# Optimization experiments

Hardware: AMD Instinct MI355X
Metric: run time of the kernel (lower is better)

## Reference

```python
import jax, jax.numpy as jnp
import numpy as np

N = 50000       # nodes
E = 800000      # edges
IN = 128        # in_channels
HID = 64        # hidden_channels
OUT = 32        # out_channels
H = 4           # heads
EH = 64         # edge_hidden_channels
EOUT = 2        # edge_out_channels
NEG_SLOPE = 0.2 # PyG GATConv default


def gat_conv(x, edge_index, W, att_src, att_dst, bias, num_nodes):
    """PyG GATConv, concat=False, add_self_loops=False, eval mode (no dropout).
    edge_attr is ignored because edge_dim=None (lin_edge is None in PyG).
    Returns (out [N, C], alpha [E, H])."""
    heads, C = att_src.shape
    xl = (x @ W).reshape(-1, heads, C)                 # [N, H, C]
    src, dst = edge_index[0], edge_index[1]
    a_src = jnp.sum(xl * att_src, axis=-1)             # [N, H]
    a_dst = jnp.sum(xl * att_dst, axis=-1)             # [N, H]
    alpha = jax.nn.leaky_relu(a_src[src] + a_dst[dst], NEG_SLOPE)  # [E, H]
    # segment softmax over destination nodes
    amax = jax.ops.segment_max(alpha, dst, num_segments=num_nodes)
    amax = jnp.where(jnp.isfinite(amax), amax, 0.0)
    ex = jnp.exp(alpha - amax[dst])
    denom = jax.ops.segment_sum(ex, dst, num_segments=num_nodes)
    alpha_n = ex / (denom[dst] + 1e-16)                # [E, H]
    msg = xl[src] * alpha_n[:, :, None]                # [E, H, C]
    out = jax.ops.segment_sum(msg, dst, num_segments=num_nodes)  # [N, H, C]
    out = out.mean(axis=1) + bias                      # concat=False -> head mean
    return out, alpha_n


def setup_inputs() -> dict:
    key = jax.random.key(0)
    ks = jax.random.split(key, 16)
    x = jax.random.normal(ks[0], (N, IN), dtype=jnp.float32)
    edge_index = jax.random.randint(ks[1], (2, E), 0, N, dtype=jnp.int32)
    edge_attr = jax.random.normal(ks[2], (E, 5), dtype=jnp.float32)
    s = lambda fan: 1.0 / np.sqrt(fan)
    W1 = jax.random.normal(ks[3], (IN, H * HID), dtype=jnp.float32) * s(IN)
    att1_src = jax.random.normal(ks[4], (H, HID), dtype=jnp.float32) * s(HID)
    att1_dst = jax.random.normal(ks[5], (H, HID), dtype=jnp.float32) * s(HID)
    b1 = jnp.zeros((HID,), dtype=jnp.float32)
    W3 = jax.random.normal(ks[6], (HID, H * OUT), dtype=jnp.float32) * s(HID)
    att3_src = jax.random.normal(ks[7], (H, OUT), dtype=jnp.float32) * s(OUT)
    att3_dst = jax.random.normal(ks[8], (H, OUT), dtype=jnp.float32) * s(OUT)
    b3 = jnp.zeros((OUT,), dtype=jnp.float32)
    EIN = 2 * OUT + H  # cat(out_src, alpha, out_dst)
    mW1 = jax.random.normal(ks[9], (EIN, EH), dtype=jnp.float32) * s(EIN)
    mb1 = jnp.zeros((EH,), dtype=jnp.float32)
    mW2 = jax.random.normal(ks[10], (EH, EOUT), dtype=jnp.float32) * s(EH)
    mb2 = jnp.zeros((EOUT,), dtype=jnp.float32)
    return {"x": x, "edge_index": edge_index, "edge_attr": edge_attr,
            "return_attention_weights": 1,
            "W1": W1, "att1_src": att1_src, "att1_dst": att1_dst, "b1": b1,
            "W3": W3, "att3_src": att3_src, "att3_dst": att3_dst, "b3": b3,
            "mW1": mW1, "mb1": mb1, "mW2": mW2, "mb2": mb2}


def reference(x, edge_index, edge_attr, return_attention_weights,
              W1, att1_src, att1_dst, b1, W3, att3_src, att3_dst, b3,
              mW1, mb1, mW2, mb2):
    edge_len = edge_attr.shape[0]  # == E (no self loops added)
    out, alpha = gat_conv(x, edge_index, W1, att1_src, att1_dst, b1, N)
    out, alpha = gat_conv(out, edge_index, W3, att3_src, att3_dst, b3, N)
    # F.dropout with training=False is the identity (eval mode)
    ei = edge_index[:, :edge_len]
    al = alpha[:edge_len, :]
    out_src = out[ei[0]]                                # [E, OUT]
    out_dst = out[ei[1]]                                # [E, OUT]
    edge_feat = jnp.concatenate([out_src, al, out_dst], axis=-1)  # [E, 2*OUT+H]
    h = jax.nn.relu(edge_feat @ mW1 + mb1)
    edge_out = h @ mW2 + mb2                            # [E, EOUT]
    return (out, edge_out)
```

## Files before the change

kernel.cpp:

```cpp
#include <hip/hip_runtime.h>
#include <hip/hip_fp16.h>

constexpr int NN   = 50000;
constexpr int EE   = 800000;
constexpr int INF  = 128;
constexpr int NH   = 4;

struct __align__(8) h4 { __half2 a, b; };

__device__ __forceinline__ float elw(float a) {
    a = (a > 0.f) ? a : 0.2f * a;
    return __expf(a);
}

__global__ __launch_bounds__(256) void gemm_pq_half(const float* __restrict__ A,
                                                    const float* __restrict__ B,
                                                    __half* __restrict__ C,
                                                    int N, int K, int M) {
    __shared__ float As[16][68];
    __shared__ float Bs[16][64];
    const int tid = threadIdx.x;
    const int tx = tid & 15, ty = tid >> 4;
    const int row0 = blockIdx.x * 64, col0 = blockIdx.y * 64;

    float acc[4][4] = {};

    for (int k0 = 0; k0 < K; k0 += 16) {
        {
            const int a_row = tid >> 2;
            const int a_k   = (tid & 3) * 4;
            const int gr    = row0 + a_row;
            float4 v = make_float4(0.f, 0.f, 0.f, 0.f);
            if (gr < N) v = *(const float4*)(A + (size_t)gr * K + k0 + a_k);
            As[a_k + 0][a_row] = v.x;
            As[a_k + 1][a_row] = v.y;
            As[a_k + 2][a_row] = v.z;
            As[a_k + 3][a_row] = v.w;
        }
        {
            const int b_k = tid >> 4;
            const int b_c = (tid & 15) * 4;
            float4 w = *(const float4*)(B + (size_t)(k0 + b_k) * M + col0 + b_c);
            *(float4*)&Bs[b_k][b_c] = w;
        }
        __syncthreads();
        #pragma unroll
        for (int kk = 0; kk < 16; ++kk) {
            float4 a = *(const float4*)&As[kk][ty * 4];
            float4 b = *(const float4*)&Bs[kk][tx * 4];
            const float av[4] = {a.x, a.y, a.z, a.w};
            const float bv[4] = {b.x, b.y, b.z, b.w};
            #pragma unroll
            for (int i = 0; i < 4; ++i)
                #pragma unroll
                for (int j = 0; j < 4; ++j)
                    acc[i][j] = fmaf(av[i], bv[j], acc[i][j]);
        }
        __syncthreads();
    }
    #pragma unroll
    for (int i = 0; i < 4; ++i) {
        const int r = row0 + ty * 4 + i;
        if (r < N) {
            __half* cp = C + (size_t)r * M + col0 + tx * 4;
            __half2 q0 = __halves2half2(__float2half_rn(acc[i][0]), __float2half_rn(acc[i][1]));
            __half2 q1 = __halves2half2(__float2half_rn(acc[i][2]), __float2half_rn(acc[i][3]));
            *(__half2*)cp       = q0;
            *(__half2*)(cp + 2) = q1;
        }
    }
}

template <int CH, bool HOUT>
__global__ __launch_bounds__(256) void gemm_att(const float* __restrict__ A,
                                                const float* __restrict__ B,
                                                void* __restrict__ Cv,
                                                const float* __restrict__ att_s,
                                                const float* __restrict__ att_d,
                                                float* __restrict__ a_s,
                                                float* __restrict__ a_d,
                                                int N, int K, int M) {
    __shared__ float As[16][68];
    __shared__ float Bs[16][64];
    const int tid = threadIdx.x;
    const int tx = tid & 15, ty = tid >> 4;
    const int row0 = blockIdx.x * 64, col0 = blockIdx.y * 64;

    const int col  = col0 + tx * 4;
    const int head = col / CH;
    const int pos  = col % CH;
    float attS[4], attD[4];
    #pragma unroll
    for (int j = 0; j < 4; ++j) {
        attS[j] = att_s[head * CH + pos + j];
        attD[j] = att_d[head * CH + pos + j];
    }

    float acc[4][4] = {};

    for (int k0 = 0; k0 < K; k0 += 16) {
        {
            const int a_row = tid >> 2;
            const int a_k   = (tid & 3) * 4;
            const int gr    = row0 + a_row;
            float4 v = make_float4(0.f, 0.f, 0.f, 0.f);
            if (gr < N) v = *(const float4*)(A + (size_t)gr * K + k0 + a_k);
            As[a_k + 0][a_row] = v.x;
            As[a_k + 1][a_row] = v.y;
            As[a_k + 2][a_row] = v.z;
            As[a_k + 3][a_row] = v.w;
        }
        {
            const int b_k = tid >> 4;
            const int b_c = (tid & 15) * 4;
            float4 w = *(const float4*)(B + (size_t)(k0 + b_k) * M + col0 + b_c);
            *(float4*)&Bs[b_k][b_c] = w;
        }
        __syncthreads();
        #pragma unroll
        for (int kk = 0; kk < 16; ++kk) {
            float4 a = *(const float4*)&As[kk][ty * 4];
            float4 b = *(const float4*)&Bs[kk][tx * 4];
            const float av[4] = {a.x, a.y, a.z, a.w};
            const float bv[4] = {b.x, b.y, b.z, b.w};
            #pragma unroll
            for (int i = 0; i < 4; ++i)
                #pragma unroll
                for (int j = 0; j < 4; ++j)
                    acc[i][j] = fmaf(av[i], bv[j], acc[i][j]);
        }
        __syncthreads();
    }
    #pragma unroll
    for (int i = 0; i < 4; ++i) {
        const int r = row0 + ty * 4 + i;
        if (r < N) {
            if constexpr (HOUT) {
                __half* C  = (__half*)Cv;
                __half* cp = C + (size_t)r * M + col0 + tx * 4;
                __half2 q0 = __halves2half2(__float2half_rn(acc[i][0]), __float2half_rn(acc[i][1]));
                __half2 q1 = __halves2half2(__float2half_rn(acc[i][2]), __float2half_rn(acc[i][3]));
                *(__half2*)cp       = q0;
                *(__half2*)(cp + 2) = q1;
            } else {
                float* C  = (float*)Cv;
                float* cp = C + (size_t)r * M + col0 + tx * 4;
                cp[0] = acc[i][0]; cp[1] = acc[i][1]; cp[2] = acc[i][2]; cp[3] = acc[i][3];
            }
        }
        float ss = 0.f, sd = 0.f;
        #pragma unroll
        for (int j = 0; j < 4; ++j) {
            ss = fmaf(acc[i][j], attS[j], ss);
            sd = fmaf(acc[i][j], attD[j], sd);
        }
        #pragma unroll
        for (int msk = 1; msk < CH / 4; msk <<= 1) {
            ss += __shfl_xor(ss, msk, 64);
            sd += __shfl_xor(sd, msk, 64);
        }
        if ((tx & (CH / 4 - 1)) == 0 && r < N) {
            a_s[r * NH + head] = ss;
            a_d[r * NH + head] = sd;
        }
    }
}

__global__ __launch_bounds__(256) void count_deg_k(const int* __restrict__ ei,
                                                   int* __restrict__ deg) {
    const int e = blockIdx.x * 256 + threadIdx.x;
    if (e < EE) atomicAdd(&deg[ei[EE + e]], 1);
}

__global__ __launch_bounds__(1024) void scan_k(const int* __restrict__ deg,
                                               int* __restrict__ rowptr,
                                               int* __restrict__ cursor) {
    __shared__ int wsum[16];
    const int tid = threadIdx.x;
    const int lane = tid & 63, wv = tid >> 6;
    int total = 0;
    for (int base = 0; base < NN; base += 1024) {
        const int i = base + tid;
        const int v = (i < NN) ? deg[i] : 0;
        int incl = v;
        #pragma unroll
        for (int d = 1; d < 64; d <<= 1) {
            int t = __shfl_up(incl, d, 64);
            if (lane >= d) incl += t;
        }
        if (lane == 63) wsum[wv] = incl;
        __syncthreads();
        if (wv == 0) {
            int s = (lane < 16) ? wsum[lane] : 0;
            #pragma unroll
            for (int d = 1; d < 16; d <<= 1) {
                int t = __shfl_up(s, d, 64);
                if (lane >= d) s += t;
            }
            if (lane < 16) wsum[lane] = s;
        }
        __syncthreads();
        const int excl = total + (wv > 0 ? wsum[wv - 1] : 0) + incl - v;
        const int chunk = wsum[15];
        if (i < NN) { rowptr[i] = excl; cursor[i] = excl; }
        total += chunk;
        __syncthreads();
    }
    if (tid == 0) rowptr[NN] = total;
}

__global__ __launch_bounds__(256) void scatter_perm_k(const int* __restrict__ ei,
                                                      int* __restrict__ cursor,
                                                      int* __restrict__ perm,
                                                      int* __restrict__ psrc,
                                                      int* __restrict__ pdst) {
    const int e = blockIdx.x * 256 + threadIdx.x;
    if (e >= EE) return;
    const int d = ei[EE + e];
    const int p = atomicAdd(&cursor[d], 1);
    perm[p] = e;
    psrc[p] = ei[e];
    pdst[p] = d;
}

__global__ __launch_bounds__(256) void softagg1h(const int* __restrict__ rowptr,
                                                 const int* __restrict__ psrc,
                                                 const float* __restrict__ a_s,
                                                 const float* __restrict__ a_d,
                                                 const __half* __restrict__ xl,
                                                 const float* __restrict__ bias,
                                                 float* __restrict__ out) {
    const int wv = threadIdx.x >> 6, lane = threadIdx.x & 63;
    const int n = blockIdx.x * 4 + wv;
    if (n >= NN) return;
    const int r0 = rowptr[n], r1 = rowptr[n + 1];
    const int hh = lane >> 4;
    const float ad = a_d[n * NH + hh];

    const h4* X = (const h4*)xl;
    float4 A0 = {0,0,0,0}, A1 = {0,0,0,0}, A2 = {0,0,0,0}, A3 = {0,0,0,0};
    float sum = 0.f;
    int j = r0;
    for (; j + 7 < r1; j += 8) {
        const int s0 = psrc[j],     s1 = psrc[j + 1], s2 = psrc[j + 2], s3 = psrc[j + 3];
        const int s4 = psrc[j + 4], s5 = psrc[j + 5], s6 = psrc[j + 6], s7 = psrc[j + 7];
        const float w0 = elw(a_s[s0 * NH + hh] + ad);
        const float w1 = elw(a_s[s1 * NH + hh] + ad);
        const float w2 = elw(a_s[s2 * NH + hh] + ad);
        const float w3 = elw(a_s[s3 * NH + hh] + ad);
        const float w4 = elw(a_s[s4 * NH + hh] + ad);
        const float w5 = elw(a_s[s5 * NH + hh] + ad);
        const float w6 = elw(a_s[s6 * NH + hh] + ad);
        const float w7 = elw(a_s[s7 * NH + hh] + ad);
        sum += ((w0 + w1) + (w2 + w3)) + ((w4 + w5) + (w6 + w7));
        const h4 v0 = X[(size_t)s0 * 64 + lane];
        const h4 v1 = X[(size_t)s1 * 64 + lane];
        const h4 v2 = X[(size_t)s2 * 64 + lane];
        const h4 v3 = X[(size_t)s3 * 64 + lane];
        const h4 v4 = X[(size_t)s4 * 64 + lane];
        const h4 v5 = X[(size_t)s5 * 64 + lane];
        const h4 v6 = X[(size_t)s6 * 64 + lane];
        const h4 v7 = X[(size_t)s7 * 64 + lane];
        float2 l0 = __half22float2(v0.a), m0 = __half22float2(v0.b);
        float2 l1 = __half22float2(v1.a), m1 = __half22float2(v1.b);
        float2 l2 = __half22float2(v2.a), m2 = __half22float2(v2.b);
        float2 l3 = __half22float2(v3.a), m3 = __half22float2(v3.b);
        float2 l4 = __half22float2(v4.a), m4 = __half22float2(v4.b);
        float2 l5 = __half22float2(v5.a), m5 = __half22float2(v5.b);
        float2 l6 = __half22float2(v6.a), m6 = __half22float2(v6.b);
        float2 l7 = __half22float2(v7.a), m7 = __half22float2(v7.b);
        A0.x = fmaf(w0, l0.x, A0.x); A0.y = fmaf(w0, l0.y, A0.y);
        A0.z = fmaf(w0, m0.x, A0.z); A0.w = fmaf(w0, m0.y, A0.w);
        A1.x = fmaf(w1, l1.x, A1.x); A1.y = fmaf(w1, l1.y, A1.y);
        A1.z = fmaf(w1, m1.x, A1.z); A1.w = fmaf(w1, m1.y, A1.w);
        A2.x = fmaf(w2, l2.x, A2.x); A2.y = fmaf(w2, l2.y, A2.y);
        A2.z = fmaf(w2, m2.x, A2.z); A2.w = fmaf(w2, m2.y, A2.w);
        A3.x = fmaf(w3, l3.x, A3.x); A3.y = fmaf(w3, l3.y, A3.y);
        A3.z = fmaf(w3, m3.x, A3.z); A3.w = fmaf(w3, m3.y, A3.w);
        A0.x = fmaf(w4, l4.x, A0.x); A0.y = fmaf(w4, l4.y, A0.y);
        A0.z = fmaf(w4, m4.x, A0.z); A0.w = fmaf(w4, m4.y, A0.w);
        A1.x = fmaf(w5, l5.x, A1.x); A1.y = fmaf(w5, l5.y, A1.y);
        A1.z = fmaf(w5, m5.x, A1.z); A1.w = fmaf(w5, m5.y, A1.w);
        A2.x = fmaf(w6, l6.x, A2.x); A2.y = fmaf(w6, l6.y, A2.y);
        A2.z = fmaf(w6, m6.x, A2.z); A2.w = fmaf(w6, m6.y, A2.w);
        A3.x = fmaf(w7, l7.x, A3.x); A3.y = fmaf(w7, l7.y, A3.y);
        A3.z = fmaf(w7, m7.x, A3.z); A3.w = fmaf(w7, m7.y, A3.w);
    }
    for (; j < r1; ++j) {
        const int s0 = psrc[j];
        const float w0 = elw(a_s[s0 * NH + hh] + ad);
        sum += w0;
        const h4 v0 = X[(size_t)s0 * 64 + lane];
        float2 l0 = __half22float2(v0.a), m0 = __half22float2(v0.b);
        A0.x = fmaf(w0, l0.x, A0.x); A0.y = fmaf(w0, l0.y, A0.y);
        A0.z = fmaf(w0, m0.x, A0.z); A0.w = fmaf(w0, m0.y, A0.w);
    }
    const float inv = 1.f / (sum + 1e-30f);
    float4 t;
    t.x = ((A0.x + A1.x) + (A2.x + A3.x)) * inv;
    t.y = ((A0.y + A1.y) + (A2.y + A3.y)) * inv;
    t.z = ((A0.z + A1.z) + (A2.z + A3.z)) * inv;
    t.w = ((A0.w + A1.w) + (A2.w + A3.w)) * inv;
    #pragma unroll
    for (int msk = 16; msk < 64; msk <<= 1) {
        t.x += __shfl_xor(t.x, msk, 64);
        t.y += __shfl_xor(t.y, msk, 64);
        t.z += __shfl_xor(t.z, msk, 64);
        t.w += __shfl_xor(t.w, msk, 64);
    }
    if (lane < 16) {
        const float4 b = ((const float4*)bias)[lane];
        float4 o;
        o.x = t.x * 0.25f + b.x; o.y = t.y * 0.25f + b.y;
        o.z = t.z * 0.25f + b.z; o.w = t.w * 0.25f + b.w;
        ((float4*)out)[(size_t)n * 16 + lane] = o;
    }
}

__global__ __launch_bounds__(256) void softagg2h(const int* __restrict__ rowptr,
                                                 const int* __restrict__ psrc,
                                                 const float* __restrict__ a_s,
                                                 const float* __restrict__ a_d,
                                                 float* __restrict__ alpha_p,
                                                 float* __restrict__ inv_s,
                                                 const __half* __restrict__ xl,
                                                 const float* __restrict__ bias,
                                                 float* __restrict__ out) {
    const int wv = threadIdx.x >> 6, lane = threadIdx.x & 63;
    const int n = blockIdx.x * 4 + wv;
    if (n >= NN) return;
    const int r0 = rowptr[n], r1 = rowptr[n + 1];
    const int cl = lane & 31, half = lane >> 5, hh = cl >> 3;
    const float ad = a_d[n * NH + hh];
    const bool writer = (cl & 7) == 0;

    const h4* X = (const h4*)xl;
    float4 A0 = {0,0,0,0}, A1 = {0,0,0,0};
    float sum = 0.f;
    int j = r0;
    for (; j + 7 < r1; j += 8) {
        const int ja = j + half, jc = j + 2 + half, je = j + 4 + half, jg = j + 6 + half;
        const int sa = psrc[ja], sc = psrc[jc], se = psrc[je], sg = psrc[jg];
        const float wa = elw(a_s[sa * NH + hh] + ad);
        const float wc = elw(a_s[sc * NH + hh] + ad);
        const float we = elw(a_s[se * NH + hh] + ad);
        const float wg = elw(a_s[sg * NH + hh] + ad);
        if (writer) {
            alpha_p[ja * NH + hh] = wa; alpha_p[jc * NH + hh] = wc;
            alpha_p[je * NH + hh] = we; alpha_p[jg * NH + hh] = wg;
        }
        sum += (wa + wc) + (we + wg);
        const h4 va = X[(size_t)sa * 32 + cl];
        const h4 vc = X[(size_t)sc * 32 + cl];
        const h4 ve = X[(size_t)se * 32 + cl];
        const h4 vg = X[(size_t)sg * 32 + cl];
        const float2 la = __half22float2(va.a), ma = __half22float2(va.b);
        const float2 lc = __half22float2(vc.a), mc = __half22float2(vc.b);
        const float2 le = __half22float2(ve.a), me = __half22float2(ve.b);
        const float2 lg = __half22float2(vg.a), mg = __half22float2(vg.b);
        A0.x = fmaf(wa, la.x, A0.x); A0.y = fmaf(wa, la.y, A0.y);
        A0.z = fmaf(wa, ma.x, A0.z); A0.w = fmaf(wa, ma.y, A0.w);
        A1.x = fmaf(wc, lc.x, A1.x); A1.y = fmaf(wc, lc.y, A1.y);
        A1.z = fmaf(wc, mc.x, A1.z); A1.w = fmaf(wc, mc.y, A1.w);
        A0.x = fmaf(we, le.x, A0.x); A0.y = fmaf(we, le.y, A0.y);
        A0.z = fmaf(we, me.x, A0.z); A0.w = fmaf(we, me.y, A0.w);
        A1.x = fmaf(wg, lg.x, A1.x); A1.y = fmaf(wg, lg.y, A1.y);
        A1.z = fmaf(wg, mg.x, A1.z); A1.w = fmaf(wg, mg.y, A1.w);
    }
    for (; j < r1; j += 2) {
        const int ja = j + half;
        const bool valid = ja < r1;
        const int sa = psrc[valid ? ja : r0];
        float wa = 0.f;
        if (valid) {
            wa = elw(a_s[sa * NH + hh] + ad);
            if (writer) alpha_p[ja * NH + hh] = wa;
        }
        sum += wa;
        const h4 va = X[(size_t)sa * 32 + cl];
        const float2 la = __half22float2(va.a), ma = __half22float2(va.b);
        A0.x = fmaf(wa, la.x, A0.x); A0.y = fmaf(wa, la.y, A0.y);
        A0.z = fmaf(wa, ma.x, A0.z); A0.w = fmaf(wa, ma.y, A0.w);
    }
    sum += __shfl_xor(sum, 32, 64);
    const float inv = 1.f / (sum + 1e-30f);
    if (writer && half == 0) inv_s[n * NH + hh] = inv;

    float4 t;
    t.x = A0.x + A1.x; t.y = A0.y + A1.y; t.z = A0.z + A1.z; t.w = A0.w + A1.w;
    t.x += __shfl_xor(t.x, 32, 64);
    t.y += __shfl_xor(t.y, 32, 64);
    t.z += __shfl_xor(t.z, 32, 64);
    t.w += __shfl_xor(t.w, 32, 64);
    t.x *= inv; t.y *= inv; t.z *= inv; t.w *= inv;
    #pragma unroll
    for (int q = 0; q < 2; ++q) {
        const int msk = (q == 0) ? 8 : 16;
        t.x += __shfl_xor(t.x, msk, 64);
        t.y += __shfl_xor(t.y, msk, 64);
        t.z += __shfl_xor(t.z, msk, 64);
        t.w += __shfl_xor(t.w, msk, 64);
    }
    if (lane < 8) {
        const float4 b = ((const float4*)bias)[lane];
        float4 o;
        o.x = t.x * 0.25f + b.x; o.y = t.y * 0.25f + b.y;
        o.z = t.z * 0.25f + b.z; o.w = t.w * 0.25f + b.w;
        ((float4*)out)[(size_t)n * 8 + lane] = o;
    }
}

__global__ __launch_bounds__(256) void pack_w1(const float* __restrict__ mW1,
                                               float* __restrict__ W1pq) {
    const int idx = blockIdx.x * 256 + threadIdx.x;
    if (idx >= 32 * 128) return;
    const int k = idx >> 7, j = idx & 127;
    W1pq[idx] = (j < 64) ? mW1[k * 64 + j] : mW1[(36 + k) * 64 + (j - 64)];
}

__global__ __launch_bounds__(256) void edge_mlp_fast2(const __half* __restrict__ PQ,
                                                      const float* __restrict__ alpha_p,
                                                      const float* __restrict__ inv_s,
                                                      const int* __restrict__ psrc,
                                                      const int* __restrict__ pdst,
                                                      const int* __restrict__ perm,
                                                      const float* __restrict__ mW1,
                                                      const float* __restrict__ mb1,
                                                      const float* __restrict__ mW2,
                                                      const float* __restrict__ mb2,
                                                      float* __restrict__ out) {
    const int lane = threadIdx.x & 63, wv = threadIdx.x >> 6;
    const int g = lane >> 4, c = lane & 15;

    const float4 wa0 = *(const float4*)&mW1[32 * 64 + c * 4];
    const float4 wa1 = *(const float4*)&mW1[33 * 64 + c * 4];
    const float4 wa2 = *(const float4*)&mW1[34 * 64 + c * 4];
    const float4 wa3 = *(const float4*)&mW1[35 * 64 + c * 4];
    const float4 b1v = *(const float4*)&mb1[c * 4];
    const float4 w2a = *(const float4*)&mW2[c * 8];
    const float4 w2b = *(const float4*)&mW2[c * 8 + 4];
    const float bo0 = mb2[0], bo1 = mb2[1];

    const h4* PQ4 = (const h4*)PQ;
    const int gw = blockIdx.x * 4 + wv;
    const int stride4 = gridDim.x * 4 * 4;

    for (int jb = gw * 4; jb < EE; jb += stride4) {
        const int j = jb + g;
        const int s = psrc[j];
        const int d = pdst[j];
        const float4 ar = *(const float4*)&alpha_p[(size_t)j * 4];
        const float4 iv = *(const float4*)&inv_s[(size_t)d * 4];
        const float al0 = ar.x * iv.x, al1 = ar.y * iv.y;
        const float al2 = ar.z * iv.z, al3 = ar.w * iv.w;
        const h4 ph = PQ4[(size_t)s * 32 + c];
        const h4 qh = PQ4[(size_t)d * 32 + 16 + c];
        const float2 pl = __half22float2(ph.a), pm = __half22float2(ph.b);
        const float2 ql = __half22float2(qh.a), qm = __half22float2(qh.b);
        float4 h;
        h.x = pl.x + ql.x + b1v.x; h.y = pl.y + ql.y + b1v.y;
        h.z = pm.x + qm.x + b1v.z; h.w = pm.y + qm.y + b1v.w;
        h.x = fmaf(al0, wa0.x, h.x); h.y = fmaf(al0, wa0.y, h.y);
        h.z = fmaf(al0, wa0.z, h.z); h.w = fmaf(al0, wa0.w, h.w);
        h.x = fmaf(al1, wa1.x, h.x); h.y = fmaf(al1, wa1.y, h.y);
        h.z = fmaf(al1, wa1.z, h.z); h.w = fmaf(al1, wa1.w, h.w);
        h.x = fmaf(al2, wa2.x, h.x); h.y = fmaf(al2, wa2.y, h.y);
        h.z = fmaf(al2, wa2.z, h.z); h.w = fmaf(al2, wa2.w, h.w);
        h.x = fmaf(al3, wa3.x, h.x); h.y = fmaf(al3, wa3.y, h.y);
        h.z = fmaf(al3, wa3.z, h.z); h.w = fmaf(al3, wa3.w, h.w);
        h.x = fmaxf(h.x, 0.f); h.y = fmaxf(h.y, 0.f);
        h.z = fmaxf(h.z, 0.f); h.w = fmaxf(h.w, 0.f);

        float v0 = h.x * w2a.x + h.y * w2a.z + h.z * w2b.x + h.w * w2b.z;
        float v1 = h.x * w2a.y + h.y * w2a.w + h.z * w2b.y + h.w * w2b.w;
        #pragma unroll
        for (int msk = 1; msk < 16; msk <<= 1) {
            v0 += __shfl_xor(v0, msk, 64);
            v1 += __shfl_xor(v1, msk, 64);
        }
        if (c == 0)
            *(float2*)&out[(size_t)perm[j] * 2] = make_float2(v0 + bo0, v1 + bo1);
    }
}

extern "C" void kernel_launch(void* const* d_in, const int* in_sizes, int n_in,
                              void* d_out, int out_size, void* d_ws, size_t ws_size,
                              hipStream_t stream) {
    const float* x        = (const float*)d_in[0];
    const int*   ei       = (const int*)d_in[1];
    const float* W1       = (const float*)d_in[4];
    const float* att1_src = (const float*)d_in[5];
    const float* att1_dst = (const float*)d_in[6];
    const float* b1       = (const float*)d_in[7];
    const float* W3       = (const float*)d_in[8];
    const float* att3_src = (const float*)d_in[9];
    const float* att3_dst = (const float*)d_in[10];
    const float* b3       = (const float*)d_in[11];
    const float* mW1      = (const float*)d_in[12];
    const float* mb1      = (const float*)d_in[13];
    const float* mW2      = (const float*)d_in[14];
    const float* mb2      = (const float*)d_in[15];

    float* out_nodes = (float*)d_out;
    float* out_edges = out_nodes + (size_t)NN * 32;

    float* ws = (float*)d_ws;
    __half*   xlh     = (__half*)ws;
    __half*   xl2h    = (__half*)ws;
    __half*   PQh     = (__half*)ws;
    float*    h1      = ws + 12800000;
    float*    alpha_p = ws + 16000000;
    float*    a_s     = ws + 25600000;
    float*    a_d     = ws + 25800000;
    float*    W1pq    = ws + 26000000;
    float*    inv_s   = ws + 26100000;
    int*      deg     = (int*)(ws + 26400000);
    int*      cursor  = (int*)(ws + 26450000);
    int*      rowptr  = (int*)(ws + 26500000);
    int*      perm    = (int*)(ws + 26550008);
    int*      psrc    = (int*)(ws + 27350008);
    int*      pdst    = (int*)(ws + 28150008);

    const int gemmRows = (NN + 63) / 64;
    const int EB = (EE + 255) / 256;
    const int NB4 = (NN + 3) / 4;

    hipMemsetAsync(deg, 0, (size_t)NN * 4, stream);
    count_deg_k<<<EB, 256, 0, stream>>>(ei, deg);
    scan_k<<<1, 1024, 0, stream>>>(deg, rowptr, cursor);
    scatter_perm_k<<<EB, 256, 0, stream>>>(ei, cursor, perm, psrc, pdst);
    pack_w1<<<16, 256, 0, stream>>>(mW1, W1pq);

    gemm_att<64, true><<<dim3(gemmRows, 4), 256, 0, stream>>>(x, W1, xlh, att1_src, att1_dst,
                                                              a_s, a_d, NN, INF, NH * 64);
    softagg1h<<<NB4, 256, 0, stream>>>(rowptr, psrc, a_s, a_d, xlh, b1, h1);

    gemm_att<32, true><<<dim3(gemmRows, 2), 256, 0, stream>>>(h1, W3, xl2h, att3_src, att3_dst,
                                                              a_s, a_d, NN, 64, NH * 32);
    softagg2h<<<NB4, 256, 0, stream>>>(rowptr, psrc, a_s, a_d, alpha_p, inv_s, xl2h, b3,
                                       out_nodes);

    gemm_pq_half<<<dim3(gemmRows, 2), 256, 0, stream>>>(out_nodes, W1pq, PQh, NN, 32, 128);
    edge_mlp_fast2<<<2048, 256, 0, stream>>>(PQh, alpha_p, inv_s, psrc, pdst, perm,
                                             mW1, mb1, mW2, mb2, out_edges);
}
```

Measured before the change: 482.7 us.

## Fuse GAT pipeline into single cooperative persistent kernel with grid syncs

Replaces the chain of separate kernel launches (degree count, scan, scatter, weight pack, two GEMM+attention stages, two softmax aggregations, PQ GEMM, edge MLP) with one cooperative kernel that separates phases with grid-wide barriers. The single-block prefix scan becomes a multi-block scan that writes per-chunk sums and then per-chunk offsets. The edge permutation scatter now runs in the same phase as the first GEMM. The aim is to remove launch gaps and the serial scan. In exchange it adds grid-sync cost, and the launch bound of four blocks per CU may constrain registers across all phases. The old multi-kernel path is kept as a fallback.

```diff
diff --git a/kernel.cpp b/kernel.cpp
--- a/kernel.cpp
+++ b/kernel.cpp
@@ -1,10 +1,15 @@
 #include <hip/hip_runtime.h>
 #include <hip/hip_fp16.h>
+#include <hip/hip_cooperative_groups.h>
+
+namespace cg = cooperative_groups;
 
 constexpr int NN   = 50000;
 constexpr int EE   = 800000;
 constexpr int INF  = 128;
 constexpr int NH   = 4;
+constexpr int GEMM_ROWS = (NN + 63) / 64;
+constexpr int NCH  = (NN + 255) / 256;
 
 struct __align__(8) h4 { __half2 a, b; };
 
@@ -13,79 +18,19 @@
     return __expf(a);
 }
 
-__global__ __launch_bounds__(256) void gemm_pq_half(const float* __restrict__ A,
-                                                    const float* __restrict__ B,
-                                                    __half* __restrict__ C,
-                                                    int N, int K, int M) {
-    __shared__ float As[16][68];
-    __shared__ float Bs[16][64];
-    const int tid = threadIdx.x;
+
+template <int CH, bool HOUT>
+__device__ __forceinline__ void gemm_att_tile(const float* __restrict__ A,
+                                              const float* __restrict__ B,
+                                              void* __restrict__ Cv,
+                                              const float* __restrict__ att_s,
+                                              const float* __restrict__ att_d,
+                                              float* __restrict__ a_s,
+                                              float* __restrict__ a_d,
+                                              int N, int K, int M,
+                                              int row0, int col0, int tid,
+                                              float (*As)[68], float (*Bs)[64]) {
     const int tx = tid & 15, ty = tid >> 4;
-    const int row0 = blockIdx.x * 64, col0 = blockIdx.y * 64;
-
-    float acc[4][4] = {};
-
-    for (int k0 = 0; k0 < K; k0 += 16) {
-        {
-            const int a_row = tid >> 2;
-            const int a_k   = (tid & 3) * 4;
-            const int gr    = row0 + a_row;
-            float4 v = make_float4(0.f, 0.f, 0.f, 0.f);
-            if (gr < N) v = *(const float4*)(A + (size_t)gr * K + k0 + a_k);
-            As[a_k + 0][a_row] = v.x;
-            As[a_k + 1][a_row] = v.y;
-            As[a_k + 2][a_row] = v.z;
-            As[a_k + 3][a_row] = v.w;
-        }
-        {
-            const int b_k = tid >> 4;
-            const int b_c = (tid & 15) * 4;
-            float4 w = *(const float4*)(B + (size_t)(k0 + b_k) * M + col0 + b_c);
-            *(float4*)&Bs[b_k][b_c] = w;
-        }
-        __syncthreads();
-        #pragma unroll
-        for (int kk = 0; kk < 16; ++kk) {
-            float4 a = *(const float4*)&As[kk][ty * 4];
-            float4 b = *(const float4*)&Bs[kk][tx * 4];
-            const float av[4] = {a.x, a.y, a.z, a.w};
-            const float bv[4] = {b.x, b.y, b.z, b.w};
-            #pragma unroll
-            for (int i = 0; i < 4; ++i)
-                #pragma unroll
-                for (int j = 0; j < 4; ++j)
-                    acc[i][j] = fmaf(av[i], bv[j], acc[i][j]);
-        }
-        __syncthreads();
-    }
-    #pragma unroll
-    for (int i = 0; i < 4; ++i) {
-        const int r = row0 + ty * 4 + i;
-        if (r < N) {
-            __half* cp = C + (size_t)r * M + col0 + tx * 4;
-            __half2 q0 = __halves2half2(__float2half_rn(acc[i][0]), __float2half_rn(acc[i][1]));
-            __half2 q1 = __halves2half2(__float2half_rn(acc[i][2]), __float2half_rn(acc[i][3]));
-            *(__half2*)cp       = q0;
-            *(__half2*)(cp + 2) = q1;
-        }
-    }
-}
-
-template <int CH, bool HOUT>
-__global__ __launch_bounds__(256) void gemm_att(const float* __restrict__ A,
-                                                const float* __restrict__ B,
-                                                void* __restrict__ Cv,
-                                                const float* __restrict__ att_s,
-                                                const float* __restrict__ att_d,
-                                                float* __restrict__ a_s,
-                                                float* __restrict__ a_d,
-                                                int N, int K, int M) {
-    __shared__ float As[16][68];
-    __shared__ float Bs[16][64];
-    const int tid = threadIdx.x;
-    const int tx = tid & 15, ty = tid >> 4;
-    const int row0 = blockIdx.x * 64, col0 = blockIdx.y * 64;
-
     const int col  = col0 + tx * 4;
     const int head = col / CH;
     const int pos  = col % CH;
@@ -95,9 +40,7 @@
         attS[j] = att_s[head * CH + pos + j];
         attD[j] = att_d[head * CH + pos + j];
     }
-
     float acc[4][4] = {};
-
     for (int k0 = 0; k0 < K; k0 += 16) {
         {
             const int a_row = tid >> 2;
@@ -166,73 +109,68 @@
     }
 }
 
-__global__ __launch_bounds__(256) void count_deg_k(const int* __restrict__ ei,
-                                                   int* __restrict__ deg) {
-    const int e = blockIdx.x * 256 + threadIdx.x;
-    if (e < EE) atomicAdd(&deg[ei[EE + e]], 1);
-}
-
-__global__ __launch_bounds__(1024) void scan_k(const int* __restrict__ deg,
-                                               int* __restrict__ rowptr,
-                                               int* __restrict__ cursor) {
-    __shared__ int wsum[16];
-    const int tid = threadIdx.x;
-    const int lane = tid & 63, wv = tid >> 6;
-    int total = 0;
-    for (int base = 0; base < NN; base += 1024) {
-        const int i = base + tid;
-        const int v = (i < NN) ? deg[i] : 0;
-        int incl = v;
+__device__ __forceinline__ void gemm_pq_tile(const float* __restrict__ A,
+                                             const float* __restrict__ B,
+                                             __half* __restrict__ C,
+                                             int N, int K, int M,
+                                             int row0, int col0, int tid,
+                                             float (*As)[68], float (*Bs)[64]) {
+    const int tx = tid & 15, ty = tid >> 4;
+    float acc[4][4] = {};
+    for (int k0 = 0; k0 < K; k0 += 16) {
+        {
+            const int a_row = tid >> 2;
+            const int a_k   = (tid & 3) * 4;
+            const int gr    = row0 + a_row;
+            float4 v = make_float4(0.f, 0.f, 0.f, 0.f);
+            if (gr < N) v = *(const float4*)(A + (size_t)gr * K + k0 + a_k);
+            As[a_k + 0][a_row] = v.x;
+            As[a_k + 1][a_row] = v.y;
+            As[a_k + 2][a_row] = v.z;
+            As[a_k + 3][a_row] = v.w;
+        }
+        {
+            const int b_k = tid >> 4;
+            const int b_c = (tid & 15) * 4;
+            float4 w = *(const float4*)(B + (size_t)(k0 + b_k) * M + col0 + b_c);
+            *(float4*)&Bs[b_k][b_c] = w;
+        }
+        __syncthreads();
         #pragma unroll
-        for (int d = 1; d < 64; d <<= 1) {
-            int t = __shfl_up(incl, d, 64);
-            if (lane >= d) incl += t;
-        }
-        if (lane == 63) wsum[wv] = incl;
-        __syncthreads();
-        if (wv == 0) {
-            int s = (lane < 16) ? wsum[lane] : 0;
+        for (int kk = 0; kk < 16; ++kk) {
+            float4 a = *(const float4*)&As[kk][ty * 4];
+            float4 b = *(const float4*)&Bs[kk][tx * 4];
+            const float av[4] = {a.x, a.y, a.z, a.w};
+            const float bv[4] = {b.x, b.y, b.z, b.w};
             #pragma unroll
-            for (int d = 1; d < 16; d <<= 1) {
-                int t = __shfl_up(s, d, 64);
-                if (lane >= d) s += t;
-            }
-            if (lane < 16) wsum[lane] = s;
-        }
-        __syncthreads();
-        const int excl = total + (wv > 0 ? wsum[wv - 1] : 0) + incl - v;
-        const int chunk = wsum[15];
-        if (i < NN) { rowptr[i] = excl; cursor[i] = excl; }
-        total += chunk;
-        __syncthreads();
-    }
-    if (tid == 0) rowptr[NN] = total;
-}
-
-__global__ __launch_bounds__(256) void scatter_perm_k(const int* __restrict__ ei,
-                                                      int* __restrict__ cursor,
-                                                      int* __restrict__ perm,
-                                                      int* __restrict__ psrc,
-                                                      int* __restrict__ pdst) {
-    const int e = blockIdx.x * 256 + threadIdx.x;
-    if (e >= EE) return;
-    const int d = ei[EE + e];
-    const int p = atomicAdd(&cursor[d], 1);
-    perm[p] = e;
-    psrc[p] = ei[e];
-    pdst[p] = d;
-}
-
-__global__ __launch_bounds__(256) void softagg1h(const int* __restrict__ rowptr,
-                                                 const int* __restrict__ psrc,
-                                                 const float* __restrict__ a_s,
-                                                 const float* __restrict__ a_d,
-                                                 const __half* __restrict__ xl,
-                                                 const float* __restrict__ bias,
-                                                 float* __restrict__ out) {
-    const int wv = threadIdx.x >> 6, lane = threadIdx.x & 63;
-    const int n = blockIdx.x * 4 + wv;
-    if (n >= NN) return;
+            for (int i = 0; i < 4; ++i)
+                #pragma unroll
+                for (int j = 0; j < 4; ++j)
+                    acc[i][j] = fmaf(av[i], bv[j], acc[i][j]);
+        }
+        __syncthreads();
+    }
+    #pragma unroll
+    for (int i = 0; i < 4; ++i) {
+        const int r = row0 + ty * 4 + i;
+        if (r < N) {
+            __half* cp = C + (size_t)r * M + col0 + tx * 4;
+            __half2 q0 = __halves2half2(__float2half_rn(acc[i][0]), __float2half_rn(acc[i][1]));
+            __half2 q1 = __halves2half2(__float2half_rn(acc[i][2]), __float2half_rn(acc[i][3]));
+            *(__half2*)cp       = q0;
+            *(__half2*)(cp + 2) = q1;
+        }
+    }
+}
+
+__device__ __forceinline__ void softagg1_node(int n, int lane,
+                                              const int* __restrict__ rowptr,
+                                              const int* __restrict__ psrc,
+                                              const float* __restrict__ a_s,
+                                              const float* __restrict__ a_d,
+                                              const __half* __restrict__ xl,
+                                              const float* __restrict__ bias,
+                                              float* __restrict__ out) {
     const int r0 = rowptr[n], r1 = rowptr[n + 1];
     const int hh = lane >> 4;
     const float ad = a_d[n * NH + hh];
@@ -317,18 +255,16 @@
     }
 }
 
-__global__ __launch_bounds__(256) void softagg2h(const int* __restrict__ rowptr,
-                                                 const int* __restrict__ psrc,
-                                                 const float* __restrict__ a_s,
-                                                 const float* __restrict__ a_d,
-                                                 float* __restrict__ alpha_p,
-                                                 float* __restrict__ inv_s,
-                                                 const __half* __restrict__ xl,
-                                                 const float* __restrict__ bias,
-                                                 float* __restrict__ out) {
-    const int wv = threadIdx.x >> 6, lane = threadIdx.x & 63;
-    const int n = blockIdx.x * 4 + wv;
-    if (n >= NN) return;
+__device__ __forceinline__ void softagg2_node(int n, int lane,
+                                              const int* __restrict__ rowptr,
+                                              const int* __restrict__ psrc,
+                                              const float* __restrict__ a_s,
+                                              const float* __restrict__ a_d,
+                                              float* __restrict__ alpha_p,
+                                              float* __restrict__ inv_s,
+                                              const __half* __restrict__ xl,
+                                              const float* __restrict__ bias,
+                                              float* __restrict__ out) {
     const int r0 = rowptr[n], r1 = rowptr[n + 1];
     const int cl = lane & 31, half = lane >> 5, hh = cl >> 3;
     const float ad = a_d[n * NH + hh];
@@ -410,26 +346,317 @@
     }
 }
 
-__global__ __launch_bounds__(256) void pack_w1(const float* __restrict__ mW1,
-                                               float* __restrict__ W1pq) {
+__global__ __launch_bounds__(256, 4) void fused_gat(
+    const float* x, const int* ei,
+    const float* W1, const float* att1s, const float* att1d, const float* b1,
+    const float* W3, const float* att3s, const float* att3d, const float* b3,
+    const float* mW1, const float* mb1, const float* mW2, const float* mb2,
+    float* out_nodes, float* out_edges,
+    __half* xlh, float* h1, __half* xl2h, __half* PQh,
+    float* alpha_p, float* a_s, float* a_d, float* W1pq, float* inv_s,
+    int* deg, int* cursor, int* rowptr, int* perm, int* psrc, int* pdst,
+    int* bsum, int* boff) {
+    cg::grid_group grid = cg::this_grid();
+    const int tid = threadIdx.x;
+    const int bid = blockIdx.x;
+    const int nB  = gridDim.x;
+    const int gtid = bid * 256 + tid;
+    const int gstride = nB * 256;
+    const int lane = tid & 63, wv = tid >> 6;
+
+    __shared__ float As[16][68];
+    __shared__ float Bs[16][64];
+    __shared__ int   sw[8];
+
+    for (int i = gtid; i < NN; i += gstride) deg[i] = 0;
+    for (int i = gtid; i < 32 * 128; i += gstride) {
+        const int k = i >> 7, jj = i & 127;
+        W1pq[i] = (jj < 64) ? mW1[k * 64 + jj] : mW1[(36 + k) * 64 + (jj - 64)];
+    }
+    grid.sync();
+
+    for (int e = gtid; e < EE; e += gstride) atomicAdd(&deg[ei[EE + e]], 1);
+    grid.sync();
+
+    for (int c = bid; c < NCH; c += nB) {
+        const int i = c * 256 + tid;
+        int s = (i < NN) ? deg[i] : 0;
+        #pragma unroll
+        for (int d = 1; d < 64; d <<= 1) s += __shfl_xor(s, d, 64);
+        if (lane == 0) sw[wv] = s;
+        __syncthreads();
+        if (tid == 0) bsum[c] = sw[0] + sw[1] + sw[2] + sw[3];
+        __syncthreads();
+    }
+    grid.sync();
+
+    if (bid == 0) {
+        int v = (tid < NCH) ? bsum[tid] : 0;
+        int incl = v;
+        #pragma unroll
+        for (int d = 1; d < 64; d <<= 1) {
+            int t = __shfl_up(incl, d, 64);
+            if (lane >= d) incl += t;
+        }
+        if (lane == 63) sw[wv] = incl;
+        __syncthreads();
+        if (wv == 0 && lane < 4) {
+            int s4 = sw[lane];
+            #pragma unroll
+            for (int d = 1; d < 4; d <<= 1) {
+                int t = __shfl_up(s4, d, 64);
+                if (lane >= d) s4 += t;
+            }
+            sw[lane + 4] = s4;
+        }
+        __syncthreads();
+        const int woff = (wv > 0) ? sw[wv - 1 + 4] : 0;
+        if (tid < NCH) boff[tid] = woff + incl - v;
+    }
+    grid.sync();
+
+    for (int c = bid; c < NCH; c += nB) {
+        const int i = c * 256 + tid;
+        int v = (i < NN) ? deg[i] : 0;
+        int incl = v;
+        #pragma unroll
+        for (int d = 1; d < 64; d <<= 1) {
+            int t = __shfl_up(incl, d, 64);
+            if (lane >= d) incl += t;
+        }
+        if (lane == 63) sw[wv] = incl;
+        __syncthreads();
+        if (wv == 0 && lane < 4) {
+            int s4 = sw[lane];
+            #pragma unroll
+            for (int d = 1; d < 4; d <<= 1) {
+                int t = __shfl_up(s4, d, 64);
+                if (lane >= d) s4 += t;
+            }
+            sw[lane + 4] = s4;
+        }
+        __syncthreads();
+        const int excl = boff[c] + ((wv > 0) ? sw[wv - 1 + 4] : 0) + incl - v;
+        if (i < NN) { rowptr[i] = excl; cursor[i] = excl; }
+        __syncthreads();
+    }
+    if (gtid == 0) rowptr[NN] = EE;
+    grid.sync();
+
+    for (int e = gtid; e < EE; e += gstride) {
+        const int dd = ei[EE + e];
+        const int p = atomicAdd(&cursor[dd], 1);
+        perm[p] = e;
+        psrc[p] = ei[e];
+        pdst[p] = dd;
+    }
+    for (int t = bid; t < GEMM_ROWS * 4; t += nB)
+        gemm_att_tile<64, true>(x, W1, xlh, att1s, att1d, a_s, a_d,
+                                NN, INF, NH * 64,
+                                (t % GEMM_ROWS) * 64, (t / GEMM_ROWS) * 64, tid, As, Bs);
+    grid.sync();
+
+    for (int n = bid * 4 + wv; n < NN; n += nB * 4)
+        softagg1_node(n, lane, rowptr, psrc, a_s, a_d, xlh, b1, h1);
+    grid.sync();
+
+    for (int t = bid; t < GEMM_ROWS * 2; t += nB)
+        gemm_att_tile<32, true>(h1, W3, xl2h, att3s, att3d, a_s, a_d,
+                                NN, 64, NH * 32,
+                                (t % GEMM_ROWS) * 64, (t / GEMM_ROWS) * 64, tid, As, Bs);
+    grid.sync();
+
+    for (int n = bid * 4 + wv; n < NN; n += nB * 4)
+        softagg2_node(n, lane, rowptr, psrc, a_s, a_d, alpha_p, inv_s, xl2h, b3, out_nodes);
+    grid.sync();
+
+    for (int t = bid; t < GEMM_ROWS * 2; t += nB)
+        gemm_pq_tile(out_nodes, W1pq, PQh, NN, 32, 128,
+                     (t % GEMM_ROWS) * 64, (t / GEMM_ROWS) * 64, tid, As, Bs);
+    grid.sync();
+
+    {
+        const int g = lane >> 4, c = lane & 15;
+        const float4 wa0 = *(const float4*)&mW1[32 * 64 + c * 4];
+        const float4 wa1 = *(const float4*)&mW1[33 * 64 + c * 4];
+        const float4 wa2 = *(const float4*)&mW1[34 * 64 + c * 4];
+        const float4 wa3 = *(const float4*)&mW1[35 * 64 + c * 4];
+        const float4 b1v = *(const float4*)&mb1[c * 4];
+        const float4 w2a = *(const float4*)&mW2[c * 8];
+        const float4 w2b = *(const float4*)&mW2[c * 8 + 4];
+        const float bo0 = mb2[0], bo1 = mb2[1];
+
+        const h4* PQ4 = (const h4*)PQh;
+        const int gw = bid * 4 + wv;
+        const int stride4 = nB * 4 * 4;
+
+        for (int jb = gw * 4; jb < EE; jb += stride4) {
+            const int j = jb + g;
+            const int s = psrc[j];
+            const int d = pdst[j];
+            const float4 ar = *(const float4*)&alpha_p[(size_t)j * 4];
+            const float4 iv = *(const float4*)&inv_s[(size_t)d * 4];
+            const float al0 = ar.x * iv.x, al1 = ar.y * iv.y;
+            const float al2 = ar.z * iv.z, al3 = ar.w * iv.w;
+            const h4 ph = PQ4[(size_t)s * 32 + c];
+            const h4 qh = PQ4[(size_t)d * 32 + 16 + c];
+            const float2 pl = __half22float2(ph.a), pm = __half22float2(ph.b);
+            const float2 ql = __half22float2(qh.a), qm = __half22float2(qh.b);
+            float4 h;
+            h.x = pl.x + ql.x + b1v.x; h.y = pl.y + ql.y + b1v.y;
+            h.z = pm.x + qm.x + b1v.z; h.w = pm.y + qm.y + b1v.w;
+            h.x = fmaf(al0, wa0.x, h.x); h.y = fmaf(al0, wa0.y, h.y);
+            h.z = fmaf(al0, wa0.z, h.z); h.w = fmaf(al0, wa0.w, h.w);
+            h.x = fmaf(al1, wa1.x, h.x); h.y = fmaf(al1, wa1.y, h.y);
+            h.z = fmaf(al1, wa1.z, h.z); h.w = fmaf(al1, wa1.w, h.w);
+            h.x = fmaf(al2, wa2.x, h.x); h.y = fmaf(al2, wa2.y, h.y);
+            h.z = fmaf(al2, wa2.z, h.z); h.w = fmaf(al2, wa2.w, h.w);
+            h.x = fmaf(al3, wa3.x, h.x); h.y = fmaf(al3, wa3.y, h.y);
+            h.z = fmaf(al3, wa3.z, h.z); h.w = fmaf(al3, wa3.w, h.w);
+            h.x = fmaxf(h.x, 0.f); h.y = fmaxf(h.y, 0.f);
+            h.z = fmaxf(h.z, 0.f); h.w = fmaxf(h.w, 0.f);
+
+            float v0 = h.x * w2a.x + h.y * w2a.z + h.z * w2b.x + h.w * w2b.z;
+            float v1 = h.x * w2a.y + h.y * w2a.w + h.z * w2b.y + h.w * w2b.w;
+            #pragma unroll
+            for (int msk = 1; msk < 16; msk <<= 1) {
+                v0 += __shfl_xor(v0, msk, 64);
+                v1 += __shfl_xor(v1, msk, 64);
+            }
+            if (c == 0)
+                *(float2*)&out_edges[(size_t)perm[j] * 2] = make_float2(v0 + bo0, v1 + bo1);
+        }
+    }
+}
+
+
+__global__ __launch_bounds__(256) void gemm_pq_half_k(const float* __restrict__ A,
+                                                      const float* __restrict__ B,
+                                                      __half* __restrict__ C,
+                                                      int N, int K, int M) {
+    __shared__ float As[16][68];
+    __shared__ float Bs[16][64];
+    gemm_pq_tile(A, B, C, N, K, M, blockIdx.x * 64, blockIdx.y * 64, threadIdx.x, As, Bs);
+}
+
+template <int CH, bool HOUT>
+__global__ __launch_bounds__(256) void gemm_att_k(const float* __restrict__ A,
+                                                  const float* __restrict__ B,
+                                                  void* __restrict__ Cv,
+                                                  const float* __restrict__ att_s,
+                                                  const float* __restrict__ att_d,
+                                                  float* __restrict__ a_s,
+                                                  float* __restrict__ a_d,
+                                                  int N, int K, int M) {
+    __shared__ float As[16][68];
+    __shared__ float Bs[16][64];
+    gemm_att_tile<CH, HOUT>(A, B, Cv, att_s, att_d, a_s, a_d, N, K, M,
+                            blockIdx.x * 64, blockIdx.y * 64, threadIdx.x, As, Bs);
+}
+
+__global__ __launch_bounds__(256) void count_deg_k(const int* __restrict__ ei,
+                                                   int* __restrict__ deg) {
+    const int e = blockIdx.x * 256 + threadIdx.x;
+    if (e < EE) atomicAdd(&deg[ei[EE + e]], 1);
+}
+
+__global__ __launch_bounds__(1024) void scan_k(const int* __restrict__ deg,
+                                               int* __restrict__ rowptr,
+                                               int* __restrict__ cursor) {
+    __shared__ int wsum[16];
+    const int tid = threadIdx.x;
+    const int lane = tid & 63, wvv = tid >> 6;
+    int total = 0;
+    for (int base = 0; base < NN; base += 1024) {
+        const int i = base + tid;
+        const int v = (i < NN) ? deg[i] : 0;
+        int incl = v;
+        #pragma unroll
+        for (int d = 1; d < 64; d <<= 1) {
+            int t = __shfl_up(incl, d, 64);
+            if (lane >= d) incl += t;
+        }
+        if (lane == 63) wsum[wvv] = incl;
+        __syncthreads();
+        if (wvv == 0) {
+            int s = (lane < 16) ? wsum[lane] : 0;
+            #pragma unroll
+            for (int d = 1; d < 16; d <<= 1) {
+                int t = __shfl_up(s, d, 64);
+                if (lane >= d) s += t;
+            }
+            if (lane < 16) wsum[lane] = s;
+        }
+        __syncthreads();
+        const int excl = total + (wvv > 0 ? wsum[wvv - 1] : 0) + incl - v;
+        const int chunk = wsum[15];
+        if (i < NN) { rowptr[i] = excl; cursor[i] = excl; }
+        total += chunk;
+        __syncthreads();
+    }
+    if (tid == 0) rowptr[NN] = total;
+}
+
+__global__ __launch_bounds__(256) void scatter_perm_k(const int* __restrict__ ei,
+                                                      int* __restrict__ cursor,
+                                                      int* __restrict__ perm,
+                                                      int* __restrict__ psrc,
+                                                      int* __restrict__ pdst) {
+    const int e = blockIdx.x * 256 + threadIdx.x;
+    if (e >= EE) return;
+    const int d = ei[EE + e];
+    const int p = atomicAdd(&cursor[d], 1);
+    perm[p] = e;
+    psrc[p] = ei[e];
+    pdst[p] = d;
+}
+
+__global__ __launch_bounds__(256) void pack_w1_k(const float* __restrict__ mW1,
+                                                 float* __restrict__ W1pq) {
     const int idx = blockIdx.x * 256 + threadIdx.x;
     if (idx >= 32 * 128) return;
     const int k = idx >> 7, j = idx & 127;
     W1pq[idx] = (j < 64) ? mW1[k * 64 + j] : mW1[(36 + k) * 64 + (j - 64)];
 }
 
-__global__ __launch_bounds__(256) void edge_mlp_fast2(const __half* __restrict__ PQ,
-                                                      const float* __restrict__ alpha_p,
-                                                      const float* __restrict__ inv_s,
-                                                      const int* __restrict__ psrc,
-                                                      const int* __restrict__ pdst,
-                                                      const int* __restrict__ perm,
-                                                      const float* __restrict__ mW1,
-                                                      const float* __restrict__ mb1,
-                                                      const float* __restrict__ mW2,
-                                                      const float* __restrict__ mb2,
-                                                      float* __restrict__ out) {
-    const int lane = threadIdx.x & 63, wv = threadIdx.x >> 6;
+__global__ __launch_bounds__(256) void softagg1h_k(const int* __restrict__ rowptr,
+                                                   const int* __restrict__ psrc,
+                                                   const float* __restrict__ a_s,
+                                                   const float* __restrict__ a_d,
+                                                   const __half* __restrict__ xl,
+                                                   const float* __restrict__ bias,
+                                                   float* __restrict__ out) {
+    const int n = blockIdx.x * 4 + (threadIdx.x >> 6);
+    if (n >= NN) return;
+    softagg1_node(n, threadIdx.x & 63, rowptr, psrc, a_s, a_d, xl, bias, out);
+}
+
+__global__ __launch_bounds__(256) void softagg2h_k(const int* __restrict__ rowptr,
+                                                   const int* __restrict__ psrc,
+                                                   const float* __restrict__ a_s,
+                                                   const float* __restrict__ a_d,
+                                                   float* __restrict__ alpha_p,
+                                                   float* __restrict__ inv_s,
+                                                   const __half* __restrict__ xl,
+                                                   const float* __restrict__ bias,
+                                                   float* __restrict__ out) {
+    const int n = blockIdx.x * 4 + (threadIdx.x >> 6);
+    if (n >= NN) return;
+    softagg2_node(n, threadIdx.x & 63, rowptr, psrc, a_s, a_d, alpha_p, inv_s, xl, bias, out);
+}
+
+__global__ __launch_bounds__(256) void edge_mlp_k(const __half* __restrict__ PQ,
+                                                  const float* __restrict__ alpha_p,
+                                                  const float* __restrict__ inv_s,
+                                                  const int* __restrict__ psrc,
+                                                  const int* __restrict__ pdst,
+                                                  const int* __restrict__ perm,
+                                                  const float* __restrict__ mW1,
+                                                  const float* __restrict__ mb1,
+                                                  const float* __restrict__ mW2,
+                                                  const float* __restrict__ mb2,
+                                                  float* __restrict__ out) {
+    const int lane = threadIdx.x & 63, wvv = threadIdx.x >> 6;
     const int g = lane >> 4, c = lane & 15;
 
     const float4 wa0 = *(const float4*)&mW1[32 * 64 + c * 4];
@@ -442,7 +669,7 @@
     const float bo0 = mb2[0], bo1 = mb2[1];
 
     const h4* PQ4 = (const h4*)PQ;
-    const int gw = blockIdx.x * 4 + wv;
+    const int gw = blockIdx.x * 4 + wvv;
     const int stride4 = gridDim.x * 4 * 4;
 
     for (int jb = gw * 4; jb < EE; jb += stride4) {
@@ -514,6 +741,8 @@
     float*    a_d     = ws + 25800000;
     float*    W1pq    = ws + 26000000;
     float*    inv_s   = ws + 26100000;
+    int*      bsum    = (int*)(ws + 26300000);
+    int*      boff    = (int*)(ws + 26301000);
     int*      deg     = (int*)(ws + 26400000);
     int*      cursor  = (int*)(ws + 26450000);
     int*      rowptr  = (int*)(ws + 26500000);
@@ -521,7 +750,38 @@
     int*      psrc    = (int*)(ws + 27350008);
     int*      pdst    = (int*)(ws + 28150008);
 
-    const int gemmRows = (NN + 63) / 64;
+    static int coopGrid = -1;
+    if (coopGrid < 0) {
+        int maxB = 0;
+        hipError_t qe = hipOccupancyMaxActiveBlocksPerMultiprocessor(&maxB, fused_gat, 256, 0);
+        if (qe == hipSuccess && maxB >= 1) {
+            int g = maxB * 256;
+            if (g > 2048) g = 2048;
+            coopGrid = g;
+        } else {
+            coopGrid = 0;
+        }
+    }
+
+    if (coopGrid > 0) {
+        void* args[] = {
+            (void*)&x, (void*)&ei,
+            (void*)&W1, (void*)&att1_src, (void*)&att1_dst, (void*)&b1,
+            (void*)&W3, (void*)&att3_src, (void*)&att3_dst, (void*)&b3,
+            (void*)&mW1, (void*)&mb1, (void*)&mW2, (void*)&mb2,
+            (void*)&out_nodes, (void*)&out_edges,
+            (void*)&xlh, (void*)&h1, (void*)&xl2h, (void*)&PQh,
+            (void*)&alpha_p, (void*)&a_s, (void*)&a_d, (void*)&W1pq, (void*)&inv_s,
+            (void*)&deg, (void*)&cursor, (void*)&rowptr,
+            (void*)&perm, (void*)&psrc, (void*)&pdst,
+            (void*)&bsum, (void*)&boff};
+        hipError_t le = hipLaunchCooperativeKernel(fused_gat, dim3(coopGrid), dim3(256),
+                                                   args, 0, stream);
+        if (le == hipSuccess) return;
+        coopGrid = 0;
+    }
+
+    const int gemmRows = GEMM_ROWS;
     const int EB = (EE + 255) / 256;
     const int NB4 = (NN + 3) / 4;
 
@@ -529,18 +789,18 @@
     count_deg_k<<<EB, 256, 0, stream>>>(ei, deg);
     scan_k<<<1, 1024, 0, stream>>>(deg, rowptr, cursor);
     scatter_perm_k<<<EB, 256, 0, stream>>>(ei, cursor, perm, psrc, pdst);
-    pack_w1<<<16, 256, 0, stream>>>(mW1, W1pq);
-
-    gemm_att<64, true><<<dim3(gemmRows, 4), 256, 0, stream>>>(x, W1, xlh, att1_src, att1_dst,
-                                                              a_s, a_d, NN, INF, NH * 64);
-    softagg1h<<<NB4, 256, 0, stream>>>(rowptr, psrc, a_s, a_d, xlh, b1, h1);
-
-    gemm_att<32, true><<<dim3(gemmRows, 2), 256, 0, stream>>>(h1, W3, xl2h, att3_src, att3_dst,
-                                                              a_s, a_d, NN, 64, NH * 32);
-    softagg2h<<<NB4, 256, 0, stream>>>(rowptr, psrc, a_s, a_d, alpha_p, inv_s, xl2h, b3,
-                                       out_nodes);
-
-    gemm_pq_half<<<dim3(gemmRows, 2), 256, 0, stream>>>(out_nodes, W1pq, PQh, NN, 32, 128);
-    edge_mlp_fast2<<<2048, 256, 0, stream>>>(PQh, alpha_p, inv_s, psrc, pdst, perm,
-                                             mW1, mb1, mW2, mb2, out_edges);
-}
+    pack_w1_k<<<16, 256, 0, stream>>>(mW1, W1pq);
+
+    gemm_att_k<64, true><<<dim3(gemmRows, 4), 256, 0, stream>>>(x, W1, xlh, att1_src, att1_dst,
+                                                                a_s, a_d, NN, INF, NH * 64);
+    softagg1h_k<<<NB4, 256, 0, stream>>>(rowptr, psrc, a_s, a_d, xlh, b1, h1);
+
+    gemm_att_k<32, true><<<dim3(gemmRows, 2), 256, 0, stream>>>(h1, W3, xl2h, att3_src, att3_dst,
+                                                                a_s, a_d, NN, 64, NH * 32);
+    softagg2h_k<<<NB4, 256, 0, stream>>>(rowptr, psrc, a_s, a_d, alpha_p, inv_s, xl2h, b3,
+                                         out_nodes);
+
+    gemm_pq_half_k<<<dim3(gemmRows, 2), 256, 0, stream>>>(out_nodes, W1pq, PQh, NN, 32, 128);
+    edge_mlp_k<<<2048, 256, 0, stream>>>(PQh, alpha_p, inv_s, psrc, pdst, perm,
+                                         mW1, mb1, mW2, mb2, out_edges);
+}
```

Result: slower. 1.219 ms (+152.6%).
